# Performance work log

Hardware: AMD Instinct MI355X
Metric: run time of the kernel (lower is better)

## Reference

```python
import jax, jax.numpy as jnp
import numpy as np
import math

N, S, E, H = 4, 4096, 1024, 16
D = E // H  # head_dim = 64


def setup_inputs() -> dict:
    key = jax.random.key(0)
    ks = jax.random.split(key, 9)
    w = 1.0 / math.sqrt(E)
    mk = lambda k, shape: (jax.random.normal(k, shape, jnp.float32) * w)
    return {
        "x": jax.random.normal(ks[0], (N, S, E), jnp.float32),
        "Wq": mk(ks[1], (E, E)), "bq": mk(ks[2], (E,)),
        "Wk": mk(ks[3], (E, E)), "bk": mk(ks[4], (E,)),
        "Wv": mk(ks[5], (E, E)), "bv": mk(ks[6], (E,)),
        "Wo": mk(ks[7], (E, E)), "bo": mk(ks[8], (E,)),
    }


def reference(x, Wq, bq, Wk, bk, Wv, bv, Wo, bo):
    n, s, e = x.shape
    h, d = H, D
    scale = 1.0 / math.sqrt(d)

    def proj(W, b):
        # nn.Linear: x @ W.T + b, then view(N,S,H,D).transpose(1,2) -> (N,H,S,D)
        y = jnp.einsum('nse,fe->nsf', x, W) + b
        return y.reshape(n, s, h, d).transpose(0, 2, 1, 3)  # (N,H,S,D)

    Q = proj(Wq, bq)
    K = proj(Wk, bk)
    V = proj(Wv, bv)

    # Faithful reproduction of the source's einsum applied to ALREADY-transposed
    # (N,H,S,D) tensors: labels n,q,h,d bind to actual dims N,H,S,D, so the
    # result is (N, S, H, H) -- heads attending to heads at each position.
    scores = jnp.einsum('nqhd,nkhd->nhqk', Q, K) * scale  # (N,S,H,H)
    attn = jax.nn.softmax(scores, axis=-1)
    # Second einsum: attn labels n,h,q,l bind to N,S,H,H; V labels n,l,h,d bind
    # to N,H,S,D. Output nqhd has actual shape (N,H,S,D).
    out = jnp.einsum('nhql,nlhd->nqhd', attn, V)  # (N,H,S,D)
    out = out.reshape(n, s, e)  # scrambled flat reshape, as in the source
    return jnp.einsum('nse,fe->nsf', out, Wo) + bo
```

## Files before the change

kernel.cpp:

```cpp
#include <hip/hip_runtime.h>
#include <hip/hip_fp16.h>
#include <stddef.h>
#include <stdint.h>


typedef _Float16 f16_t;
typedef _Float16 f16x8 __attribute__((ext_vector_type(8)));
typedef _Float16 f16x4 __attribute__((ext_vector_type(4)));
typedef float    f32x4 __attribute__((ext_vector_type(4)));

static constexpr int Sdim = 4096;
static constexpr int Edim = 1024;
static constexpr int Mrows = 4 * Sdim;
static constexpr size_t MATEL = (size_t)Mrows * Edim;
static constexpr size_t WEL = (size_t)Edim * Edim;

__device__ __forceinline__ void gload_lds16(const f16_t* g, f16_t* l) {
  __builtin_amdgcn_global_load_lds(
      (const __attribute__((address_space(1))) void*)g,
      (__attribute__((address_space(3))) void*)l, 16, 0, 0);
}

__device__ __forceinline__ f16x8 ds_read16(uint32_t byte_addr) {
  f16x8 r;
  asm volatile("ds_read_b128 %0, %1" : "=v"(r) : "v"(byte_addr));
  return r;
}

#define SCHED_FENCE() __builtin_amdgcn_sched_barrier(0)

__global__ __launch_bounds__(256) void cvt_kernel(
    const float* __restrict__ s0, const float* __restrict__ s1,
    const float* __restrict__ s2, const float* __restrict__ s3,
    const float* __restrict__ s4,
    f16_t* __restrict__ d0, f16_t* __restrict__ d1, f16_t* __restrict__ d2,
    f16_t* __restrict__ d3, f16_t* __restrict__ d4) {
  const float* s; f16_t* d; size_t nv;
  switch (blockIdx.y) {
    case 0: s = s0; d = d0; nv = MATEL / 4; break;
    case 1: s = s1; d = d1; nv = WEL / 4; break;
    case 2: s = s2; d = d2; nv = WEL / 4; break;
    case 3: s = s3; d = d3; nv = WEL / 4; break;
    default: s = s4; d = d4; nv = WEL / 4; break;
  }
  const size_t stride = (size_t)gridDim.x * 256;
  for (size_t i = blockIdx.x * 256 + threadIdx.x; i < nv; i += stride) {
    const f32x4 v = ((const f32x4*)s)[i];
    f16x4 h;
#pragma unroll
    for (int j = 0; j < 4; j++) h[j] = (f16_t)v[j];
    ((f16x4*)d)[i] = h;
  }
}

static constexpr int BM2 = 256, BN2 = 256, BK2 = 64;
static constexpr int NT2 = Edim / BK2;
static constexpr int HALF2 = 128 * BK2;

template <int V> struct ic { static constexpr int v = V; };

template <typename TOut>
__device__ __forceinline__ void gemm256(const f16_t* __restrict__ A,
                                        const f16_t* __restrict__ B,
                                        const float* __restrict__ bias,
                                        TOut* __restrict__ C) {
  __shared__ __align__(16) f16_t lds[2][2][2][HALF2];

  const int t = threadIdx.x;
  const int lane = t & 63;
  const int w = t >> 6;
  const int l16 = lane & 15;
  const int quad = lane >> 4;
  const int ha = w >> 2;
  const int hb = (w & 3) >> 1;
  const int wnr = (w & 1) * 64;

  const uint32_t ldsBase = (uint32_t)(uintptr_t)
      (__attribute__((address_space(3))) f16_t*)&lds[0][0][0][0];
  const uint32_t aHalfOff = (uint32_t)(ha * (HALF2 * 2));
  const uint32_t bHalfOff = (uint32_t)(32768 + hb * (HALF2 * 2));

  const int id = blockIdx.x;
  const int id2 = (id & 7) * 32 + (id >> 3);
  const int bm = (id2 & 63) * BM2;
  const int bn = (id2 >> 6) * BN2;

  const int srow = w * 8 + (lane >> 3);
  const int scol = ((lane & 7) ^ ((lane >> 3) & 7)) * 8;
  const size_t gA0 = (size_t)(bm + srow) * Edim + scol;
  const size_t gB0 = (size_t)(bn + srow) * Edim + scol;
  const int lws = w * 512 + lane * 8;

  auto stage = [&](int mat, int half, int slot, int kt) {
    const f16_t* g = (mat == 0 ? A + gA0 : B + gB0) +
                     (size_t)half * 128 * Edim + kt * BK2;
    f16_t* l = &lds[slot][mat][half][lws];
    gload_lds16(g, l);
    gload_lds16(g + (size_t)64 * Edim, l + 4096);
  };

  f32x4 acc[8][4] = {};

  stage(0, 0, 0, 0); stage(0, 1, 0, 0);
  stage(1, 0, 0, 0); stage(1, 1, 0, 0);
  stage(1, 0, 1, 1); stage(1, 1, 1, 1);
  asm volatile("s_waitcnt vmcnt(4)");
  SCHED_FENCE();
  __builtin_amdgcn_s_barrier();
  SCHED_FENCE();

  auto ktile = [&](int tt, auto Sc, auto SAc, auto SBc, auto VNc) {
    constexpr int S = decltype(Sc)::v;
    constexpr int SA = decltype(SAc)::v;
    constexpr int SB = decltype(SBc)::v;
    constexpr int VN = decltype(VNc)::v;
    const uint32_t aB = ldsBase + (uint32_t)(S * 65536) + aHalfOff;
    const uint32_t bB = ldsBase + (uint32_t)(S * 65536) + bHalfOff;
    f16x8 bf[2][4];
#pragma unroll
    for (int kc = 0; kc < 2; ++kc) {
#pragma unroll
      for (int ih = 0; ih < 2; ++ih) {
        if (kc == 0) {
          const int kk = ih;
#pragma unroll
          for (int j = 0; j < 4; ++j) {
            const int r = wnr + j * 16 + l16;
            bf[kk][j] = ds_read16(
                bB + (uint32_t)((r * 64 + ((kk * 32 + quad * 8) ^
                                           ((r & 7) << 3))) * 2));
          }
        }
        f16x8 af[4];
#pragma unroll
        for (int ii = 0; ii < 4; ++ii) {
          const int r = ih * 64 + ii * 16 + l16;
          af[ii] = ds_read16(
              aB + (uint32_t)((r * 64 + ((kc * 32 + quad * 8) ^
                                         ((r & 7) << 3))) * 2));
        }
        if (kc == 0 && ih == 0) { if (SA) stage(0, 0, S ^ 1, tt + 1); }
        if (kc == 0 && ih == 1) { if (SA) stage(0, 1, S ^ 1, tt + 1); }
        if (kc == 1 && ih == 0) { if (SB) stage(1, 0, S, tt + 2); }
        if (kc == 1 && ih == 1) {
          if (SB) stage(1, 1, S, tt + 2);
          if (VN) asm volatile("s_waitcnt vmcnt(4)");
          else    asm volatile("s_waitcnt vmcnt(0)");
        }
        SCHED_FENCE();
        __builtin_amdgcn_s_barrier();
        asm volatile("s_waitcnt lgkmcnt(0)");
        SCHED_FENCE();
        __builtin_amdgcn_s_setprio(1);
#pragma unroll
        for (int ii = 0; ii < 4; ++ii)
#pragma unroll
          for (int j = 0; j < 4; ++j)
            acc[ih * 4 + ii][j] = __builtin_amdgcn_mfma_f32_16x16x32_f16(
                af[ii], bf[kc][j], acc[ih * 4 + ii][j], 0, 0, 0);
        __builtin_amdgcn_s_setprio(0);
        SCHED_FENCE();
        __builtin_amdgcn_s_barrier();
        SCHED_FENCE();
      }
    }
  };

  for (int it = 0; it < NT2 / 2 - 1; ++it) {
    ktile(2 * it,     ic<0>{}, ic<1>{}, ic<1>{}, ic<1>{});
    ktile(2 * it + 1, ic<1>{}, ic<1>{}, ic<1>{}, ic<1>{});
  }
  ktile(NT2 - 2, ic<0>{}, ic<1>{}, ic<0>{}, ic<0>{});
  ktile(NT2 - 1, ic<1>{}, ic<0>{}, ic<0>{}, ic<0>{});

  const int wm = ha * 128;
  const int wn = (w & 3) * 64;
#pragma unroll
  for (int j = 0; j < 4; ++j) {
    const int col = bn + wn + j * 16 + l16;
    const float bv = bias[col];
#pragma unroll
    for (int i = 0; i < 8; ++i) {
      const int rb = bm + wm + i * 16 + quad * 4;
#pragma unroll
      for (int r = 0; r < 4; ++r)
        C[(size_t)(rb + r) * Edim + col] = (TOut)(acc[i][j][r] + bv);
    }
  }
}

__global__ __launch_bounds__(512, 2) void qkv_kernel(
    const f16_t* __restrict__ x,
    const f16_t* __restrict__ Wq, const float* __restrict__ bq,
    const f16_t* __restrict__ Wk, const float* __restrict__ bk,
    const f16_t* __restrict__ Wv, const float* __restrict__ bv,
    f16_t* __restrict__ Qb, f16_t* __restrict__ Kb, f16_t* __restrict__ Vb) {
  const f16_t* W; const float* bi; f16_t* C;
  if (blockIdx.z == 0)      { W = Wq; bi = bq; C = Qb; }
  else if (blockIdx.z == 1) { W = Wk; bi = bk; C = Kb; }
  else                      { W = Wv; bi = bv; C = Vb; }
  gemm256<f16_t>(x, W, bi, C);
}

__global__ __launch_bounds__(512, 2) void outp_kernel(
    const f16_t* __restrict__ Ab, const f16_t* __restrict__ Wo,
    const float* __restrict__ bo, float* __restrict__ out) {
  gemm256<float>(Ab, Wo, bo, out);
}

__global__ __launch_bounds__(256) void attn_kernel(const f16_t* __restrict__ Qb,
                                                   const f16_t* __restrict__ Kb,
                                                   const f16_t* __restrict__ Vb,
                                                   f16_t* __restrict__ Ab) {
  __shared__ __align__(16) f16_t Vs[4][1024];
  const int t = threadIdx.x;
  const int w = t >> 6;
  const int lane = t & 63;
  const int l16 = lane & 15;
  const int quad = lane >> 4;
  const int pos = blockIdx.x * 4 + w;
  const int n4 = pos >> 12;
  const int s = pos & (Sdim - 1);

  const f16_t* Qr = Qb + (size_t)pos * Edim;
  const f16_t* Kr = Kb + (size_t)pos * Edim;
  const f16_t* Vr = Vb + (size_t)pos * Edim;

  *(f16x8*)&Vs[w][lane * 16]     = *(const f16x8*)(Vr + lane * 16);
  *(f16x8*)&Vs[w][lane * 16 + 8] = *(const f16x8*)(Vr + lane * 16 + 8);

  f32x4 sacc = {};
#pragma unroll
  for (int step = 0; step < 2; step++) {
    const int off = l16 * 64 + step * 32 + quad * 8;
    const f16x8 kf = *(const f16x8*)(Kr + off);
    const f16x8 qf = *(const f16x8*)(Qr + off);
    sacc = __builtin_amdgcn_mfma_f32_16x16x32_f16(kf, qf, sacc, 0, 0, 0);
  }
#pragma unroll
  for (int r = 0; r < 4; r++) sacc[r] *= 0.125f;

  float m = fmaxf(fmaxf(sacc[0], sacc[1]), fmaxf(sacc[2], sacc[3]));
  m = fmaxf(m, __shfl_xor(m, 16));
  m = fmaxf(m, __shfl_xor(m, 32));
  float e[4];
#pragma unroll
  for (int r = 0; r < 4; r++) e[r] = __expf(sacc[r] - m);
  float l = (e[0] + e[1]) + (e[2] + e[3]);
  l += __shfl_xor(l, 16);
  l += __shfl_xor(l, 32);
  const float inv = 1.0f / l;
  f16x4 pa;
#pragma unroll
  for (int r = 0; r < 4; r++) pa[r] = (f16_t)(e[r] * inv);

  __syncthreads();
  f32x4 oacc[4];
#pragma unroll
  for (int dc = 0; dc < 4; dc++) {
    f16x4 vbf;
#pragma unroll
    for (int j = 0; j < 4; j++)
      vbf[j] = Vs[w][(quad * 4 + j) * 64 + dc * 16 + l16];
    f32x4 z = {};
    oacc[dc] = __builtin_amdgcn_mfma_f32_16x16x16f16(pa, vbf, z, 0, 0, 0);
  }

  const size_t obase =
      ((size_t)(n4 << 12) + (size_t)(s >> 4)) * Edim + (size_t)(s & 15) * 64 + l16;
#pragma unroll
  for (int reg = 0; reg < 4; reg++) {
    const size_t rowoff = obase + (size_t)(quad * 4 + reg) * 256 * Edim;
#pragma unroll
    for (int dc = 0; dc < 4; dc++)
      Ab[rowoff + dc * 16] = (f16_t)oacc[dc][reg];
  }
}

extern "C" void kernel_launch(void* const* d_in, const int* in_sizes, int n_in,
                              void* d_out, int out_size, void* d_ws, size_t ws_size,
                              hipStream_t stream) {
  const float* x  = (const float*)d_in[0];
  const float* Wq = (const float*)d_in[1];
  const float* bq = (const float*)d_in[2];
  const float* Wk = (const float*)d_in[3];
  const float* bk = (const float*)d_in[4];
  const float* Wv = (const float*)d_in[5];
  const float* bv = (const float*)d_in[6];
  const float* Wo = (const float*)d_in[7];
  const float* bo = (const float*)d_in[8];
  float* out = (float*)d_out;

  f16_t* xh  = (f16_t*)d_ws;
  f16_t* Wqh = xh + MATEL;
  f16_t* Wkh = Wqh + WEL;
  f16_t* Wvh = Wkh + WEL;
  f16_t* Woh = Wvh + WEL;
  f16_t* Qb  = Woh + WEL;
  f16_t* Kb  = Qb + MATEL;
  f16_t* Vb  = Kb + MATEL;
  f16_t* Ab  = Vb + MATEL;

  cvt_kernel<<<dim3(2048, 5), dim3(256), 0, stream>>>(x, Wq, Wk, Wv, Wo,
                                                      xh, Wqh, Wkh, Wvh, Woh);
  const int ngrid = (Mrows / BM2) * (Edim / BN2);
  qkv_kernel<<<dim3(ngrid, 1, 3), dim3(512), 0, stream>>>(
      xh, Wqh, bq, Wkh, bk, Wvh, bv, Qb, Kb, Vb);
  attn_kernel<<<dim3(Mrows / 4), dim3(256), 0, stream>>>(Qb, Kb, Vb, Ab);
  outp_kernel<<<dim3(ngrid), dim3(512), 0, stream>>>(Ab, Woh, bo, out);
}
```

Before: 341.6 us.

## Software-pipeline LDS fragment reads against MFMA and cut per-tile barriers

Restructures the GEMM k-tile loop so the A/B fragment reads for the next sub-step are issued while MFMAs on the current fragments run. It uses double-buffered register fragments, partial lgkmcnt waits and a single barrier per k-tile instead of four. Launch bounds drop from 2 to 1 block per CU so the compiler can use more registers for the extra fragments. The cost is lower occupancy, and the tighter vmcnt/lgkmcnt accounting risks races if the counts are wrong.

```diff
diff --git a/kernel.cpp b/kernel.cpp
--- a/kernel.cpp
+++ b/kernel.cpp
@@ -99,79 +99,88 @@
     gload_lds16(g + (size_t)64 * Edim, l + 4096);
   };
 
+  auto rdaddr = [&](uint32_t base, int r, int c0) -> uint32_t {
+    return base + (uint32_t)((r * 64 + (c0 ^ ((r & 7) << 3))) * 2);
+  };
+
   f32x4 acc[8][4] = {};
+  f16x8 af0[4], af1[4], bf0[4], bf1[4];
+
+  auto rdA = [&](uint32_t aBase, int ih, int kc, f16x8* dst) {
+#pragma unroll
+    for (int ii = 0; ii < 4; ++ii) {
+      const int r = ih * 64 + ii * 16 + l16;
+      dst[ii] = ds_read16(rdaddr(aBase, r, kc * 32 + quad * 8));
+    }
+  };
+  auto rdB = [&](uint32_t bBase, int kc, f16x8* dst) {
+#pragma unroll
+    for (int j = 0; j < 4; ++j) {
+      const int r = wnr + j * 16 + l16;
+      dst[j] = ds_read16(rdaddr(bBase, r, kc * 32 + quad * 8));
+    }
+  };
+  auto mmac = [&](const f16x8* af, const f16x8* bf, int ih) {
+    __builtin_amdgcn_s_setprio(1);
+#pragma unroll
+    for (int ii = 0; ii < 4; ++ii)
+#pragma unroll
+      for (int j = 0; j < 4; ++j)
+        acc[ih * 4 + ii][j] = __builtin_amdgcn_mfma_f32_16x16x32_f16(
+            af[ii], bf[j], acc[ih * 4 + ii][j], 0, 0, 0);
+    __builtin_amdgcn_s_setprio(0);
+  };
 
   stage(0, 0, 0, 0); stage(0, 1, 0, 0);
   stage(1, 0, 0, 0); stage(1, 1, 0, 0);
   stage(1, 0, 1, 1); stage(1, 1, 1, 1);
-  asm volatile("s_waitcnt vmcnt(4)");
+  asm volatile("s_waitcnt vmcnt(2)");
   SCHED_FENCE();
   __builtin_amdgcn_s_barrier();
   SCHED_FENCE();
-
-  auto ktile = [&](int tt, auto Sc, auto SAc, auto SBc, auto VNc) {
-    constexpr int S = decltype(Sc)::v;
+  rdA(ldsBase + aHalfOff, 0, 0, af0);
+  rdB(ldsBase + bHalfOff, 0, bf0);
+
+  auto ktile = [&](int tt, auto SAc, auto SBc, auto NQc) {
     constexpr int SA = decltype(SAc)::v;
     constexpr int SB = decltype(SBc)::v;
-    constexpr int VN = decltype(VNc)::v;
-    const uint32_t aB = ldsBase + (uint32_t)(S * 65536) + aHalfOff;
-    const uint32_t bB = ldsBase + (uint32_t)(S * 65536) + bHalfOff;
-    f16x8 bf[2][4];
-#pragma unroll
-    for (int kc = 0; kc < 2; ++kc) {
-#pragma unroll
-      for (int ih = 0; ih < 2; ++ih) {
-        if (kc == 0) {
-          const int kk = ih;
-#pragma unroll
-          for (int j = 0; j < 4; ++j) {
-            const int r = wnr + j * 16 + l16;
-            bf[kk][j] = ds_read16(
-                bB + (uint32_t)((r * 64 + ((kk * 32 + quad * 8) ^
-                                           ((r & 7) << 3))) * 2));
-          }
-        }
-        f16x8 af[4];
-#pragma unroll
-        for (int ii = 0; ii < 4; ++ii) {
-          const int r = ih * 64 + ii * 16 + l16;
-          af[ii] = ds_read16(
-              aB + (uint32_t)((r * 64 + ((kc * 32 + quad * 8) ^
-                                         ((r & 7) << 3))) * 2));
-        }
-        if (kc == 0 && ih == 0) { if (SA) stage(0, 0, S ^ 1, tt + 1); }
-        if (kc == 0 && ih == 1) { if (SA) stage(0, 1, S ^ 1, tt + 1); }
-        if (kc == 1 && ih == 0) { if (SB) stage(1, 0, S, tt + 2); }
-        if (kc == 1 && ih == 1) {
-          if (SB) stage(1, 1, S, tt + 2);
-          if (VN) asm volatile("s_waitcnt vmcnt(4)");
-          else    asm volatile("s_waitcnt vmcnt(0)");
-        }
-        SCHED_FENCE();
-        __builtin_amdgcn_s_barrier();
-        asm volatile("s_waitcnt lgkmcnt(0)");
-        SCHED_FENCE();
-        __builtin_amdgcn_s_setprio(1);
-#pragma unroll
-        for (int ii = 0; ii < 4; ++ii)
-#pragma unroll
-          for (int j = 0; j < 4; ++j)
-            acc[ih * 4 + ii][j] = __builtin_amdgcn_mfma_f32_16x16x32_f16(
-                af[ii], bf[kc][j], acc[ih * 4 + ii][j], 0, 0, 0);
-        __builtin_amdgcn_s_setprio(0);
-        SCHED_FENCE();
-        __builtin_amdgcn_s_barrier();
-        SCHED_FENCE();
-      }
-    }
-  };
-
-  for (int it = 0; it < NT2 / 2 - 1; ++it) {
-    ktile(2 * it,     ic<0>{}, ic<1>{}, ic<1>{}, ic<1>{});
-    ktile(2 * it + 1, ic<1>{}, ic<1>{}, ic<1>{}, ic<1>{});
-  }
-  ktile(NT2 - 2, ic<0>{}, ic<1>{}, ic<0>{}, ic<0>{});
-  ktile(NT2 - 1, ic<1>{}, ic<0>{}, ic<0>{}, ic<0>{});
+    constexpr int NQ = decltype(NQc)::v;
+    const int S = tt & 1;
+    const uint32_t aB  = ldsBase + (uint32_t)(S * 65536) + aHalfOff;
+    const uint32_t bB  = ldsBase + (uint32_t)(S * 65536) + bHalfOff;
+    const uint32_t aBn = ldsBase + (uint32_t)((S ^ 1) * 65536) + aHalfOff;
+    const uint32_t bBn = ldsBase + (uint32_t)((S ^ 1) * 65536) + bHalfOff;
+    rdA(aB, 1, 0, af1);
+    if (SA) { stage(0, 0, S ^ 1, tt + 1); stage(0, 1, S ^ 1, tt + 1); }
+    SCHED_FENCE();
+    asm volatile("s_waitcnt lgkmcnt(4)");
+    SCHED_FENCE();
+    mmac(af0, bf0, 0);
+    rdA(aB, 0, 1, af0);
+    rdB(bB, 1, bf1);
+    SCHED_FENCE();
+    asm volatile("s_waitcnt lgkmcnt(8)");
+    SCHED_FENCE();
+    mmac(af1, bf0, 1);
+    rdA(aB, 1, 1, af1);
+    SCHED_FENCE();
+    asm volatile("s_waitcnt lgkmcnt(4)");
+    SCHED_FENCE();
+    mmac(af0, bf1, 0);
+    asm volatile("s_waitcnt lgkmcnt(0)");
+    asm volatile("s_waitcnt vmcnt(0)");
+    SCHED_FENCE();
+    __builtin_amdgcn_s_barrier();
+    SCHED_FENCE();
+    if (SB) { stage(1, 0, S, tt + 2); stage(1, 1, S, tt + 2); }
+    if (NQ) { rdA(aBn, 0, 0, af0); rdB(bBn, 0, bf0); }
+    SCHED_FENCE();
+    mmac(af1, bf1, 1);
+  };
+
+  for (int tt = 0; tt < NT2 - 2; ++tt) ktile(tt, ic<1>{}, ic<1>{}, ic<1>{});
+  ktile(NT2 - 2, ic<1>{}, ic<0>{}, ic<1>{});
+  ktile(NT2 - 1, ic<0>{}, ic<0>{}, ic<0>{});
 
   const int wm = ha * 128;
   const int wn = (w & 3) * 64;
@@ -189,7 +198,7 @@
   }
 }
 
-__global__ __launch_bounds__(512, 2) void qkv_kernel(
+__global__ __launch_bounds__(512, 1) void qkv_kernel(
     const f16_t* __restrict__ x,
     const f16_t* __restrict__ Wq, const float* __restrict__ bq,
     const f16_t* __restrict__ Wk, const float* __restrict__ bk,
@@ -202,7 +211,7 @@
   gemm256<f16_t>(x, W, bi, C);
 }
 
-__global__ __launch_bounds__(512, 2) void outp_kernel(
+__global__ __launch_bounds__(512, 1) void outp_kernel(
     const f16_t* __restrict__ Ab, const f16_t* __restrict__ Wo,
     const float* __restrict__ bo, float* __restrict__ out) {
   gemm256<float>(Ab, Wo, bo, out);
```

New measurement: 339.6 us. No clear change (-0.6%).
